# Performance work log

Hardware: AMD Instinct MI355X
Metric: run time of the kernel (lower is better)

## Reference

```python
import jax, jax.numpy as jnp
import numpy as np

NVAR, B, C, H, W = 3, 4, 256, 64, 64
C1 = C // 2          # dat channels (nc)
C2 = C - C1
HEADS = 4
HC = C1 // HEADS     # head channels
STRIDE = 4
KS = 4
HK, WK = H // STRIDE, W // STRIDE
NS = HK * WK         # n_sample
RPE_H, RPE_W = 2 * H - 1, 2 * W - 1
NPAIR = 3


def _grid_sample(img, grid):
    # img [B,C,Hi,Wi]; grid [B,Hg,Wg,2] = (x,y) in [-1,1]; bilinear, align_corners=True, zero-pad
    Bn, Cn, Hi, Wi = img.shape
    x = (grid[..., 0] + 1.0) * 0.5 * (Wi - 1)
    y = (grid[..., 1] + 1.0) * 0.5 * (Hi - 1)
    x0 = jnp.floor(x)
    y0 = jnp.floor(y)
    wx = x - x0
    wy = y - y0
    x0i = x0.astype(jnp.int32)
    y0i = y0.astype(jnp.int32)
    imt = img.transpose(0, 2, 3, 1)  # [B,Hi,Wi,C]
    bidx = jnp.arange(Bn)[:, None, None]

    def corner(yi, xi, wgt):
        ok = ((xi >= 0) & (xi < Wi) & (yi >= 0) & (yi < Hi)).astype(img.dtype)
        val = imt[bidx, jnp.clip(yi, 0, Hi - 1), jnp.clip(xi, 0, Wi - 1)]  # [B,Hg,Wg,C]
        return val * (wgt * ok)[..., None]

    out = (corner(y0i, x0i, (1 - wx) * (1 - wy))
           + corner(y0i, x0i + 1, wx * (1 - wy))
           + corner(y0i + 1, x0i, (1 - wx) * wy)
           + corner(y0i + 1, x0i + 1, wx * wy))
    return out.transpose(0, 3, 1, 2)  # [B,C,Hg,Wg]


def _ref_points(hk, wk):
    # normalized sampling-grid reference points, (y,x) order
    ry = (jnp.linspace(0.5, hk - 0.5, hk) / (hk - 1.0)) * 2.0 - 1.0
    rx = (jnp.linspace(0.5, wk - 0.5, wk) / (wk - 1.0)) * 2.0 - 1.0
    return jnp.stack(jnp.meshgrid(ry, rx, indexing='ij'), axis=-1)  # [hk,wk,2]


def _q_grid(h, w):
    gy = (jnp.arange(h, dtype=jnp.float32) / (h - 1.0)) * 2.0 - 1.0
    gx = (jnp.arange(w, dtype=jnp.float32) / (w - 1.0)) * 2.0 - 1.0
    return jnp.stack(jnp.meshgrid(gy, gx, indexing='ij'), axis=-1).reshape(h * w, 2)


def _conv1x1(x, w, b=None):
    y = jnp.einsum('oc,bchw->bohw', w, x)
    return y if b is None else y + b[None, :, None, None]


def _dat_block(q_in, kv_in, pWq, pbq, pWk, pbk, pWv, pbv, pWo, pbo,
               pdw_w, pdw_b, pln_g, pln_b, ppw_w, prpe):
    Bn = q_in.shape[0]
    q = _conv1x1(q_in, pWq, pbq)  # [B,C1,H,W]
    # offset net: depthwise 4x4 stride-4 conv -> channel LN -> GELU -> 1x1 conv to 2
    off = jax.lax.conv_general_dilated(
        q, pdw_w, (STRIDE, STRIDE), 'VALID',
        dimension_numbers=('NCHW', 'OIHW', 'NCHW'),
        feature_group_count=C1) + pdw_b[None, :, None, None]  # [B,C1,HK,WK]
    mu = off.mean(axis=1, keepdims=True)
    var = ((off - mu) ** 2).mean(axis=1, keepdims=True)
    off = (off - mu) * jax.lax.rsqrt(var + 1e-5) * pln_g[None, :, None, None] + pln_b[None, :, None, None]
    off = jax.nn.gelu(off, approximate=False)
    offset = _conv1x1(off, ppw_w).transpose(0, 2, 3, 1)  # [B,HK,WK,2] (dy,dx)
    # offset_range_factor = -1 -> no tanh scaling, clamp pos into [-1,1]
    pos = jnp.clip(offset + _ref_points(HK, WK)[None], -1.0, 1.0)  # [B,HK,WK,2]
    xs = _grid_sample(kv_in, pos[..., ::-1])  # sample kv at deformed points -> [B,C1,HK,WK]
    k = _conv1x1(xs, pWk, pbk).reshape(Bn, HEADS, HC, NS)
    v = _conv1x1(xs, pWv, pbv).reshape(Bn, HEADS, HC, NS)
    qh = q.reshape(Bn, HEADS, HC, H * W)
    attn = jnp.einsum('bhcm,bhcn->bhmn', qh, k) * (HC ** -0.5)  # [B,h,HW,NS]
    # relative position bias sampled from rpe table
    disp = (_q_grid(H, W)[None, :, None, :] - pos.reshape(Bn, 1, NS, 2)) * 0.5  # [B,HW,NS,2]
    rpe_b = jnp.broadcast_to(prpe[None], (Bn, HEADS, RPE_H, RPE_W))
    bias = _grid_sample(rpe_b, disp[..., ::-1])  # [B,h,HW,NS]
    attn = jax.nn.softmax(attn + bias, axis=-1)
    out = jnp.einsum('bhmn,bhcn->bhcm', attn, v).reshape(Bn, C1, H, W)
    return _conv1x1(out, pWo, pbo)


def _forward(xs, params):
    results = []
    num = 0
    for i in range(NVAR):
        res = xs[i]
        for j in range(i):
            attn_out = _dat_block(xs[i][:, :C1], xs[j][:, :C1],
                                  *(p[num] for p in params))
            # torch: res -= -cat(zeros[:,:C2], attn)  => add attn on channels C2:
            res = res.at[:, C2:].add(attn_out)
            num += 1
        results.append(res)
    return jnp.stack(results)  # [NVAR,B,C,H,W]


def setup_inputs() -> dict:
    key = jax.random.key(0)
    ks = jax.random.split(key, 4)
    d = {}
    for n, k in zip(['x0', 'x1', 'x2'], jax.random.split(ks[0], 3)):
        d[n] = jax.random.normal(k, (B, C, H, W), jnp.float32)

    def w(k, shape, s=0.02):
        return jax.random.normal(k, shape, jnp.float32) * s

    kk = jax.random.split(ks[1], 8)
    d['Wq'] = w(kk[0], (NPAIR, C1, C1))
    d['bq'] = jnp.zeros((NPAIR, C1), jnp.float32)
    d['Wk'] = w(kk[1], (NPAIR, C1, C1))
    d['bk'] = jnp.zeros((NPAIR, C1), jnp.float32)
    d['Wv'] = w(kk[2], (NPAIR, C1, C1))
    d['bv'] = jnp.zeros((NPAIR, C1), jnp.float32)
    d['Wo'] = w(kk[3], (NPAIR, C1, C1))
    d['bo'] = jnp.zeros((NPAIR, C1), jnp.float32)
    d['dw_w'] = w(kk[4], (NPAIR, C1, 1, KS, KS), 0.1)
    d['dw_b'] = jnp.zeros((NPAIR, C1), jnp.float32)
    d['ln_g'] = jnp.ones((NPAIR, C1), jnp.float32)
    d['ln_b'] = jnp.zeros((NPAIR, C1), jnp.float32)
    d['pw_w'] = w(kk[5], (NPAIR, 2, C1), 0.1)
    d['rpe'] = w(kk[6], (NPAIR, HEADS, RPE_H, RPE_W), 0.01)
    return d


def reference(x0, x1, x2, Wq, bq, Wk, bk, Wv, bv, Wo, bo,
              dw_w, dw_b, ln_g, ln_b, pw_w, rpe):
    params = (Wq, bq, Wk, bk, Wv, bv, Wo, bo, dw_w, dw_b, ln_g, ln_b, pw_w, rpe)
    out = _forward([x0, x1, x2], params)
    flow = jnp.zeros((NVAR, x0.shape[0]), out.dtype)
    return out, flow
```

## Files before the change

### kernel.cpp

```cpp
#include <hip/hip_runtime.h>
#include <math.h>

#define NVAR 3
#define BB 4
#define CC 256
#define C1 128
#define HEADS 4
#define HH 64
#define WW 64
#define HW 4096
#define RPE_W 127
#define NP 3
#define SCALE 0.17677669529663687f

typedef short bf16x8 __attribute__((ext_vector_type(8)));
typedef float f32x4 __attribute__((ext_vector_type(4)));
typedef __bf16 bf16x2 __attribute__((ext_vector_type(2)));

__device__ __forceinline__ unsigned short f2bf(float f) {
    unsigned int u = __float_as_uint(f);
    u += 0x7fffu + ((u >> 16) & 1u);
    return (unsigned short)(u >> 16);
}
__device__ __forceinline__ float bflo(unsigned u) { return __uint_as_float(u << 16); }
__device__ __forceinline__ float bfhi(unsigned u) { return __uint_as_float(u & 0xffff0000u); }

__device__ __forceinline__ float dot2bf(unsigned a, unsigned b, float c) {
#if __has_builtin(__builtin_amdgcn_fdot2_f32_bf16)
    return __builtin_amdgcn_fdot2_f32_bf16(__builtin_bit_cast(bf16x2, a),
                                           __builtin_bit_cast(bf16x2, b), c, false);
#else
    return c + bflo(a) * bflo(b) + bfhi(a) * bfhi(b);
#endif
}

__global__ __launch_bounds__(256) void prep_copy(const float* __restrict__ rpe,
                                                 const float* __restrict__ Wq,
                                                 const float* __restrict__ Wo,
                                                 const float* __restrict__ Wk,
                                                 const float* __restrict__ Wv,
                                                 const float* __restrict__ x0,
                                                 unsigned short* __restrict__ tabbf,
                                                 unsigned short* __restrict__ wqh,
                                                 unsigned short* __restrict__ woh,
                                                 unsigned short* __restrict__ wkh,
                                                 unsigned short* __restrict__ wvh,
                                                 float* __restrict__ out) {
    int blk = blockIdx.x;
    if (blk >= 24) {
        const long long n4 = (long long)BB * CC * HW / 4;
        long long i = (long long)(blk - 24) * 256 + threadIdx.x;
        const long long stride = 1024LL * 256;
        for (; i < n4 + 12; i += stride) {
            if (i < n4) ((float4*)out)[i] = ((const float4*)x0)[i];
            else out[3LL * BB * CC * HW + (i - n4)] = 0.f;
        }
        return;
    }
    if (blk < 12) {
        const float* src = rpe + (long long)blk * RPE_W * RPE_W;
        unsigned short* dst = tabbf + (long long)blk * 16384;
        for (int idx = threadIdx.x; idx < 16384; idx += 256) {
            int y = idx >> 7, x = idx & 127;
            float v = (y < RPE_W && x < RPE_W) ? src[y * RPE_W + x] : 0.f;
            dst[idx] = f2bf(v);
        }
    } else if (blk < 15) {
        int p = blk - 12;
        for (int i = threadIdx.x; i < 16384; i += 256)
            wqh[p * 16384 + i] = f2bf(Wq[p * 16384 + i]);
    } else if (blk < 18) {
        int p = blk - 15;
        for (int i = threadIdx.x; i < 16384; i += 256)
            woh[p * 16384 + i] = f2bf(Wo[p * 16384 + i]);
    } else if (blk < 21) {
        int p = blk - 18;
        for (int i = threadIdx.x; i < 16384; i += 256)
            wkh[p * 16384 + i] = f2bf(Wk[p * 16384 + i]);
    } else {
        int p = blk - 21;
        for (int i = threadIdx.x; i < 16384; i += 256)
            wvh[p * 16384 + i] = f2bf(Wv[p * 16384 + i]);
    }
}

__global__ __launch_bounds__(256) void conv_q(const float* __restrict__ x1,
                                              const float* __restrict__ x2,
                                              const unsigned short* __restrict__ wqh,
                                              const float* __restrict__ bq,
                                              unsigned short* __restrict__ qbf,
                                              float* __restrict__ out) {
    __shared__ unsigned short qlds[4][16][136];
    int wid = threadIdx.x >> 6, lane = threadIdx.x & 63;
    int g = lane >> 4, lm = lane & 15;
    int gw = blockIdx.x * 4 + wid;
    int mt = gw & 255;
    int pbi = gw >> 8;
    int merged = pbi >> 2;
    int b = pbi & 3;
    const float* X = (merged ? x2 : x1) + (long long)b * CC * HW;
    int m = mt * 16 + lm;
    int qi = merged + 1;
    float* outc = out + (((long long)(qi * 4 + b)) * CC) * HW + m;

    bf16x8 bh[4];
#pragma unroll
    for (int ksl = 0; ksl < 4; ksl++) {
        float v[8];
#pragma unroll
        for (int j = 0; j < 8; j++) {
            int k = ksl * 32 + 8 * g + j;
            v[j] = X[(long long)k * HW + m];
            outc[(long long)k * HW] = v[j];
        }
        union { unsigned u[4]; bf16x8 v; } H;
#pragma unroll
        for (int t = 0; t < 4; t++)
            H.u[t] = (unsigned)f2bf(v[2 * t]) | ((unsigned)f2bf(v[2 * t + 1]) << 16);
        bh[ksl] = H.v;
    }

    f32x4 zero = {0.f, 0.f, 0.f, 0.f};
    unsigned short* ql = &qlds[wid][lm][0];
    int qq = lane >> 4, cg = lane & 15;

    for (int rep = 0; rep <= merged; rep++) {
        int p = merged ? (1 + rep) : 0;
        int pb = p * 4 + b;
        const unsigned short* WH = wqh + p * 16384;
#pragma unroll
        for (int ct2 = 0; ct2 < 4; ct2++) {
            int ct0 = 2 * ct2, ct1 = ct0 + 1;
            f32x4 a0 = zero, a1 = zero;
#pragma unroll
            for (int ksl = 0; ksl < 4; ksl++) {
                bf16x8 Ah0 = *(const bf16x8*)(WH + (ct0 * 16 + lm) * 128 + ksl * 32 + 8 * g);
                bf16x8 Ah1 = *(const bf16x8*)(WH + (ct1 * 16 + lm) * 128 + ksl * 32 + 8 * g);
                a0 = __builtin_amdgcn_mfma_f32_16x16x32_bf16(Ah0, bh[ksl], a0, 0, 0, 0);
                a1 = __builtin_amdgcn_mfma_f32_16x16x32_bf16(Ah1, bh[ksl], a1, 0, 0, 0);
            }
            float q0[4], q1[4];
#pragma unroll
            for (int r = 0; r < 4; r++) {
                q0[r] = a0[r] + bq[p * 128 + ct0 * 16 + 4 * g + r];
                q1[r] = a1[r] + bq[p * 128 + ct1 * 16 + 4 * g + r];
            }
            *(unsigned*)(ql + ct0 * 16 + 4 * g) =
                (unsigned)f2bf(q0[0] * SCALE) | ((unsigned)f2bf(q0[1] * SCALE) << 16);
            *(unsigned*)(ql + ct0 * 16 + 4 * g + 2) =
                (unsigned)f2bf(q0[2] * SCALE) | ((unsigned)f2bf(q0[3] * SCALE) << 16);
            *(unsigned*)(ql + ct1 * 16 + 4 * g) =
                (unsigned)f2bf(q1[0] * SCALE) | ((unsigned)f2bf(q1[1] * SCALE) << 16);
            *(unsigned*)(ql + ct1 * 16 + 4 * g + 2) =
                (unsigned)f2bf(q1[2] * SCALE) | ((unsigned)f2bf(q1[3] * SCALE) << 16);
        }
        unsigned short* Yb = qbf + ((long long)pb * HW + mt * 16) * 128;
#pragma unroll
        for (int i = 0; i < 4; i++) {
            int row = i * 4 + qq;
            uint4 vv = *(const uint4*)&qlds[wid][row][cg * 8];
            *(uint4*)(Yb + row * 128 + cg * 8) = vv;
        }
    }
}

__global__ __launch_bounds__(256) void mid_kernel(const unsigned short* __restrict__ qbf,
                                                  const float* __restrict__ dw_w,
                                                  const float* __restrict__ dw_b,
                                                  const float* __restrict__ ln_g,
                                                  const float* __restrict__ ln_b,
                                                  const float* __restrict__ pw_w,
                                                  const float* __restrict__ x0,
                                                  const float* __restrict__ x1,
                                                  float* __restrict__ posb,
                                                  uint4* __restrict__ prmb,
                                                  unsigned short* __restrict__ xT) {
    __shared__ char sm[40960];
    int blk = blockIdx.x;
    int tid = threadIdx.x;
    if (blk < 192) {
        unsigned short* qs = (unsigned short*)sm;
        float (*dwout)[128] = (float(*)[128])(sm + 32768);
        int pb = blk >> 4, hk = blk & 15;
        int p = pb >> 2;
        int c = tid & 127;
        int wk0 = tid >> 7;
        const float* dwp_g = dw_w + (p * 128 + c) * 16;
        float dwp[16];
#pragma unroll
        for (int j = 0; j < 16; j++) dwp[j] = dwp_g[j] * (1.f / SCALE);
        float acc[8];
#pragma unroll
        for (int o = 0; o < 8; o++) acc[o] = dw_b[p * 128 + c];
        const unsigned short* Q = qbf + ((long long)pb * HW + hk * 256) * 128;
        for (int pass = 0; pass < 2; pass++) {
            __syncthreads();
#pragma unroll
            for (int it = 0; it < 8; it++) {
                int idx = tid + it * 256;
                int mloc = idx >> 4, cg = idx & 15;
                *(uint4*)(qs + mloc * 128 + cg * 8) =
                    *(const uint4*)(Q + (long long)(pass * 128 + mloc) * 128 + cg * 8);
            }
            __syncthreads();
#pragma unroll
            for (int o = 0; o < 8; o++) {
                int wk = wk0 + o * 2;
                float a = acc[o];
#pragma unroll
                for (int kyl = 0; kyl < 2; kyl++)
#pragma unroll
                    for (int kx = 0; kx < 4; kx++)
                        a += bflo((unsigned)qs[(kyl * 64 + wk * 4 + kx) * 128 + c])
                             * dwp[(pass * 2 + kyl) * 4 + kx];
                acc[o] = a;
            }
        }
        __syncthreads();
#pragma unroll
        for (int o = 0; o < 8; o++) dwout[wk0 + o * 2][c] = acc[o];
        __syncthreads();
        int wid = tid >> 6, lane = tid & 63;
        for (int i = 0; i < 4; i++) {
            int wk = wid * 4 + i;
            int s = hk * 16 + wk;
            float a0 = dwout[wk][lane], a1 = dwout[wk][lane + 64];
            float s1 = a0 + a1;
#pragma unroll
            for (int o = 1; o < 64; o <<= 1) s1 += __shfl_xor(s1, o);
            float mu = s1 * (1.f / 128.f);
            float d0 = a0 - mu, d1 = a1 - mu;
            float v2 = d0 * d0 + d1 * d1;
#pragma unroll
            for (int o = 1; o < 64; o <<= 1) v2 += __shfl_xor(v2, o);
            float rs = rsqrtf(v2 * (1.f / 128.f) + 1e-5f);
            int c0 = lane, c1 = lane + 64;
            float y0 = d0 * rs * ln_g[p * 128 + c0] + ln_b[p * 128 + c0];
            float y1 = d1 * rs * ln_g[p * 128 + c1] + ln_b[p * 128 + c1];
            float g0 = 0.5f * y0 * (1.f + erff(y0 * 0.70710678118654752f));
            float g1 = 0.5f * y1 * (1.f + erff(y1 * 0.70710678118654752f));
            float o0 = pw_w[(p * 2 + 0) * 128 + c0] * g0
                     + pw_w[(p * 2 + 0) * 128 + c1] * g1;
            float o1 = pw_w[(p * 2 + 1) * 128 + c0] * g0
                     + pw_w[(p * 2 + 1) * 128 + c1] * g1;
#pragma unroll
            for (int o = 1; o < 64; o <<= 1) o0 += __shfl_xor(o0, o);
#pragma unroll
            for (int o = 1; o < 64; o <<= 1) o1 += __shfl_xor(o1, o);
            if (lane == 0) {
                int wk2 = s & 15;
                float refy = (hk + 0.5f) * (2.f / 15.f) - 1.f;
                float refx = (wk2 + 0.5f) * (2.f / 15.f) - 1.f;
                float py = fminf(fmaxf(o0 + refy, -1.f), 1.f);
                float px = fminf(fmaxf(o1 + refx, -1.f), 1.f);
                int pbn = pb * 256 + s;
                posb[pbn * 2 + 0] = py;
                posb[pbn * 2 + 1] = px;
                float cy = 31.5f * (1.f - py), cx = 31.5f * (1.f - px);
                float yf = floorf(cy), xf = floorf(cx);
                float wy = cy - yf, wx = cx - xf;
                int Y0 = (int)yf, X0 = (int)xf;
                uint4 v;
                v.x = (unsigned)f2bf((1.f - wy) * (1.f - wx))
                    | ((unsigned)f2bf((1.f - wy) * wx) << 16);
                v.y = (unsigned)f2bf(wy * (1.f - wx))
                    | ((unsigned)f2bf(wy * wx) << 16);
                v.z = (unsigned)((Y0 * 128 + X0) * 2);
                v.w = 0;
                prmb[pbn] = v;
            }
        }
    } else {
        float (*ld2)[65] = (float(*)[65])sm;
        int rem = blk - 192;
        int v = rem >> 10;
        int rem1 = rem & 1023;
        int b = rem1 >> 8;
        int rem2 = rem1 & 255;
        int ct = rem2 >> 6;
        int mt = rem2 & 63;
        const float* src = ((v == 0) ? x0 : x1) + (long long)b * CC * HW
                           + (long long)(ct * 32) * HW + mt * 64;
#pragma unroll
        for (int it = 0; it < 2; it++) {
            int c = tid >> 3, x4 = (tid & 7) + it * 8;
            float4 w = *(const float4*)(src + (long long)c * HW + x4 * 4);
            ld2[c][x4 * 4 + 0] = w.x;
            ld2[c][x4 * 4 + 1] = w.y;
            ld2[c][x4 * 4 + 2] = w.z;
            ld2[c][x4 * 4 + 3] = w.w;
        }
        __syncthreads();
        int m = tid >> 2, cg = tid & 3;
        union { unsigned u[4]; } pk;
#pragma unroll
        for (int t = 0; t < 4; t++) {
            unsigned short h0 = f2bf(ld2[cg * 8 + 2 * t][m]);
            unsigned short h1 = f2bf(ld2[cg * 8 + 2 * t + 1][m]);
            pk.u[t] = (unsigned)h0 | ((unsigned)h1 << 16);
        }
        *(uint4*)(xT + (((long long)(v * 4 + b)) * HW + mt * 64 + m) * 128
                  + ct * 32 + cg * 8) = *(uint4*)pk.u;
    }
}

__global__ __launch_bounds__(256) void sample_kv(const unsigned short* __restrict__ xT,
                                                 const float* __restrict__ posb,
                                                 const unsigned short* __restrict__ wkh,
                                                 const unsigned short* __restrict__ wvh,
                                                 const float* __restrict__ bk,
                                                 const float* __restrict__ bv,
                                                 unsigned short* __restrict__ kbf,
                                                 unsigned short* __restrict__ vbf) {
    __shared__ unsigned short xls[32 * 128];
    int blk = blockIdx.x;
    int pb = blk >> 3;
    int nt = blk & 7;
    int p = pb >> 2, b = pb & 3;
    int n0 = nt * 32;
    int tid = threadIdx.x;

    {
        int nl = tid >> 3, co = tid & 7;
        int n = n0 + nl;
        float py = posb[(pb * 256 + n) * 2 + 0];
        float px = posb[(pb * 256 + n) * 2 + 1];
        float yi = (py + 1.f) * 31.5f, xi = (px + 1.f) * 31.5f;
        yi = fminf(fmaxf(yi, 0.f), 63.f);
        xi = fminf(fmaxf(xi, 0.f), 63.f);
        int y0 = min((int)yi, 62);
        int x0i = min((int)xi, 62);
        float wy = yi - (float)y0, wx = xi - (float)x0i;
        float w00 = (1.f - wy) * (1.f - wx), w01 = (1.f - wy) * wx;
        float w10 = wy * (1.f - wx), w11 = wy * wx;
        int vsel = (p == 2) ? 1 : 0;
        const unsigned short* base = xT + ((long long)(vsel * 4 + b)) * HW * 128;
        int m00 = y0 * 64 + x0i;
        char* dst = (char*)xls;
#pragma unroll
        for (int cb = 0; cb < 2; cb++) {
            int c0 = co * 16 + cb * 8;
            bf16x8 a = *(const bf16x8*)(base + (long long)m00 * 128 + c0);
            bf16x8 bb = *(const bf16x8*)(base + (long long)(m00 + 1) * 128 + c0);
            bf16x8 cc = *(const bf16x8*)(base + (long long)(m00 + 64) * 128 + c0);
            bf16x8 dd = *(const bf16x8*)(base + (long long)(m00 + 65) * 128 + c0);
            union { unsigned u[4]; bf16x8 v; } R;
#pragma unroll
            for (int t = 0; t < 4; t++) {
                float r0 = w00 * bflo((unsigned)(unsigned short)a[2 * t])
                         + w01 * bflo((unsigned)(unsigned short)bb[2 * t])
                         + w10 * bflo((unsigned)(unsigned short)cc[2 * t])
                         + w11 * bflo((unsigned)(unsigned short)dd[2 * t]);
                float r1 = w00 * bflo((unsigned)(unsigned short)a[2 * t + 1])
                         + w01 * bflo((unsigned)(unsigned short)bb[2 * t + 1])
                         + w10 * bflo((unsigned)(unsigned short)cc[2 * t + 1])
                         + w11 * bflo((unsigned)(unsigned short)dd[2 * t + 1]);
                R.u[t] = (unsigned)f2bf(r0) | ((unsigned)f2bf(r1) << 16);
            }
            *(bf16x8*)(dst + ((nl * 256 + c0 * 2) ^ ((nl & 7) << 4))) = R.v;
        }
    }
    __syncthreads();

    int wid = tid >> 6, lane = tid & 63;
    int g = lane >> 4, lm = lane & 15;
    int ntile = wid & 1, isv = wid >> 1;
    int nl = ntile * 16 + lm;
    const char* srcl = (const char*)xls;
    bf16x8 xf[4];
#pragma unroll
    for (int ks = 0; ks < 4; ks++)
        xf[ks] = *(const bf16x8*)(srcl + ((nl * 256 + (ks * 32 + 8 * g) * 2)
                                          ^ ((nl & 7) << 4)));
    f32x4 zero = {0.f, 0.f, 0.f, 0.f};
    if (!isv) {
        const unsigned short* WK = wkh + p * 16384;
#pragma unroll
        for (int ct = 0; ct < 8; ct++) {
            f32x4 acc = zero;
#pragma unroll
            for (int ks = 0; ks < 4; ks++) {
                bf16x8 wf = *(const bf16x8*)(WK + (ct * 16 + lm) * 128 + ks * 32 + 8 * g);
                acc = __builtin_amdgcn_mfma_f32_16x16x32_bf16(xf[ks], wf, acc, 0, 0, 0);
            }
            float bias = bk[p * 128 + ct * 16 + lm];
#pragma unroll
            for (int r = 0; r < 4; r++) {
                int n = n0 + ntile * 16 + 4 * g + r;
                kbf[((long long)pb * 256 + n) * 128 + ct * 16 + lm] = f2bf(acc[r] + bias);
            }
        }
    } else {
        const unsigned short* WV = wvh + p * 16384;
#pragma unroll
        for (int ct = 0; ct < 8; ct++) {
            f32x4 acc = zero;
#pragma unroll
            for (int ks = 0; ks < 4; ks++) {
                bf16x8 wf = *(const bf16x8*)(WV + (ct * 16 + lm) * 128 + ks * 32 + 8 * g);
                acc = __builtin_amdgcn_mfma_f32_16x16x32_bf16(wf, xf[ks], acc, 0, 0, 0);
            }
#pragma unroll
            for (int r = 0; r < 4; r++) {
                int c = ct * 16 + 4 * g + r;
                vbf[((long long)pb * 128 + c) * 256 + n0 + ntile * 16 + lm]
                    = f2bf(acc[r] + bv[p * 128 + c]);
            }
        }
    }
}

__global__ __launch_bounds__(512, 4) void attn_mfma(
        const unsigned short* __restrict__ qbf,
        const unsigned short* __restrict__ kbf,
        const unsigned short* __restrict__ vbf,
        const unsigned short* __restrict__ tabbf,
        const uint4* __restrict__ prmb,
        unsigned short* __restrict__ obf) {
    __shared__ unsigned short tab[16384 + 8];
    __shared__ uint4 prm[256];
    int tid = threadIdx.x;
    int wid = tid >> 6, lane = tid & 63;
    int g = lane >> 4, lm = lane & 15;
    int nh = wid >> 2;
    int mq = wid & 3;
    int bid = blockIdx.x;
    int my = bid & 63;
    int h = (bid >> 6) & 3;
    int b = (bid >> 8) & 3;
    int p = bid >> 10;
    int pb = p * 4 + b;

    {
        const uint4* ts = (const uint4*)(tabbf + (long long)(p * 4 + h) * 16384);
        uint4* td = (uint4*)tab;
#pragma unroll
        for (int i = 0; i < 4; i++) td[tid + i * 512] = ts[tid + i * 512];
        if (tid < 256) prm[tid] = prmb[pb * 256 + tid];
    }
    __syncthreads();

    int mx = (mq << 4) + lm;
    int nb = nh * 128;

    bf16x8 qf = *(const bf16x8*)(qbf + ((long long)pb * HW + my * 64 + mx) * 128
                                 + h * 32 + 8 * g);
    const unsigned short* kbase = kbf + ((long long)pb * 256 + lm) * 128
                                  + h * 32 + 8 * g;
    f32x4 zero = {0.f, 0.f, 0.f, 0.f};
    f32x4 acc[8];
    __builtin_amdgcn_s_setprio(1);
#pragma unroll
    for (int ni = 0; ni < 8; ni++) {
        bf16x8 kf = *(const bf16x8*)(kbase + (nb + ni * 16) * 128);
        acc[ni] = __builtin_amdgcn_mfma_f32_16x16x32_bf16(kf, qf, zero, 0, 0, 0);
    }
    __builtin_amdgcn_s_setprio(0);

    int laneoff = (my * 128 + mx) * 2;
    const char* tb = (const char*)tab;
#pragma unroll
    for (int ni = 0; ni < 8; ni++) {
#pragma unroll
        for (int r = 0; r < 4; r++) {
            int n = nb + ni * 16 + 4 * g + r;
            uint4 pw = prm[n];
            int va = (int)pw.z + laneoff;
            int va4 = va & ~3;
            int sh = va & 3;
            unsigned r0 = *(const unsigned*)(tb + va4);
            unsigned r1 = *(const unsigned*)(tb + va4 + 4);
            unsigned r2 = *(const unsigned*)(tb + va4 + 256);
            unsigned r3 = *(const unsigned*)(tb + va4 + 260);
            unsigned p0 = __builtin_amdgcn_alignbyte(r1, r0, sh);
            unsigned p1 = __builtin_amdgcn_alignbyte(r3, r2, sh);
            float t = acc[ni][r];
            t = dot2bf(p0, pw.x, t);
            t = dot2bf(p1, pw.y, t);
            acc[ni][r] = t;
        }
    }

    float mloc = -1e30f;
#pragma unroll
    for (int ni = 0; ni < 8; ni++)
        mloc = fmaxf(mloc, fmaxf(fmaxf(acc[ni][0], acc[ni][1]),
                                 fmaxf(acc[ni][2], acc[ni][3])));
    mloc = fmaxf(mloc, __shfl_xor(mloc, 16));
    mloc = fmaxf(mloc, __shfl_xor(mloc, 32));

    float* mex = (float*)tab;
    float* sex = (float*)tab + 128;
    float* oex = (float*)tab + 256;
    __syncthreads();
    if (g == 0) mex[nh * 64 + mx] = mloc;
    __syncthreads();
    float mglob = fmaxf(mex[mx], mex[64 + mx]);

    float lsum = 0.f;
    unsigned dwA[8], dwB[8];
#pragma unroll
    for (int ni = 0; ni < 8; ni++) {
        float e0 = __expf(acc[ni][0] - mglob);
        float e1 = __expf(acc[ni][1] - mglob);
        float e2 = __expf(acc[ni][2] - mglob);
        float e3 = __expf(acc[ni][3] - mglob);
        lsum += (e0 + e1) + (e2 + e3);
        asm("v_cvt_pk_bf16_f32 %0, %1, %2" : "=v"(dwA[ni]) : "v"(e0), "v"(e1));
        asm("v_cvt_pk_bf16_f32 %0, %1, %2" : "=v"(dwB[ni]) : "v"(e2), "v"(e3));
    }
    lsum += __shfl_xor(lsum, 16);
    lsum += __shfl_xor(lsum, 32);
    if (g == 0) sex[nh * 64 + mx] = lsum;

    int src0 = ((g & 1) << 5) + lm;
    int src1 = src0 + 16;
    bool sel = (g >> 1) != 0;
    const unsigned short* vb0 = vbf + ((long long)pb * 128 + h * 32 + lm) * 256
                                + 8 * g + nb;
    f32x4 o0 = zero, o1 = zero;
#pragma unroll
    for (int st = 0; st < 4; st++) {
        unsigned d0a = __shfl(dwA[2 * st], src0), d0b = __shfl(dwA[2 * st + 1], src0);
        unsigned d1a = __shfl(dwB[2 * st], src0), d1b = __shfl(dwB[2 * st + 1], src0);
        unsigned d2a = __shfl(dwA[2 * st], src1), d2b = __shfl(dwA[2 * st + 1], src1);
        unsigned d3a = __shfl(dwB[2 * st], src1), d3b = __shfl(dwB[2 * st + 1], src1);
        union { unsigned u[4]; bf16x8 v; } pf;
        pf.u[0] = sel ? d0b : d0a;
        pf.u[1] = sel ? d1b : d1a;
        pf.u[2] = sel ? d2b : d2a;
        pf.u[3] = sel ? d3b : d3a;
        bf16x8 v0 = *(const bf16x8*)(vb0 + st * 32);
        bf16x8 v1 = *(const bf16x8*)(vb0 + 4096 + st * 32);
        __builtin_amdgcn_s_setprio(1);
        o0 = __builtin_amdgcn_mfma_f32_16x16x32_bf16(v0, pf.v, o0, 0, 0, 0);
        o1 = __builtin_amdgcn_mfma_f32_16x16x32_bf16(v1, pf.v, o1, 0, 0, 0);
        __builtin_amdgcn_s_setprio(0);
    }

    if (nh == 1) {
        float* od = oex + (mq * 64 + lane) * 8;
#pragma unroll
        for (int r = 0; r < 4; r++) { od[r] = o0[r]; od[4 + r] = o1[r]; }
    }
    __syncthreads();
    if (nh == 1) return;

    const float* os = oex + (mq * 64 + lane) * 8;
#pragma unroll
    for (int r = 0; r < 4; r++) { o0[r] += os[r]; o1[r] += os[4 + r]; }
    float inv = 1.f / (sex[mx] + sex[64 + mx]);

    unsigned short* bounce = tab + 6144;
    {
        unsigned short* rw = bounce + mq * 640 + lm * 40;
        *(unsigned*)(rw + g * 4) =
            (unsigned)f2bf(o0[0] * inv) | ((unsigned)f2bf(o0[1] * inv) << 16);
        *(unsigned*)(rw + g * 4 + 2) =
            (unsigned)f2bf(o0[2] * inv) | ((unsigned)f2bf(o0[3] * inv) << 16);
        *(unsigned*)(rw + 16 + g * 4) =
            (unsigned)f2bf(o1[0] * inv) | ((unsigned)f2bf(o1[1] * inv) << 16);
        *(unsigned*)(rw + 16 + g * 4 + 2) =
            (unsigned)f2bf(o1[2] * inv) | ((unsigned)f2bf(o1[3] * inv) << 16);
    }
    int row = lane >> 2, cb = lane & 3;
    uint4 vv = *(const uint4*)(bounce + mq * 640 + row * 40 + cb * 8);
    *(uint4*)(obf + ((long long)pb * HW + my * 64 + mq * 16 + row) * 128
              + h * 32 + cb * 8) = vv;
}

__global__ __launch_bounds__(256) void conv_wo(const float* __restrict__ x1,
                                               const float* __restrict__ x2,
                                               const unsigned short* __restrict__ obf,
                                               const unsigned short* __restrict__ woh,
                                               const float* __restrict__ bo,
                                               float* __restrict__ out) {
    int wid = threadIdx.x >> 6, lane = threadIdx.x & 63;
    int g = lane >> 4, lm = lane & 15;
    int gw = blockIdx.x * 4 + wid;
    int mt = gw & 255;
    int b = (gw >> 8) & 3;
    int vs = gw >> 10;
    int m = mt * 16 + lm;
    int np = vs + 1;

    f32x4 acc[8];
#pragma unroll
    for (int ct = 0; ct < 8; ct++) acc[ct] = (f32x4){0.f, 0.f, 0.f, 0.f};

    for (int pi = 0; pi < np; pi++) {
        int p = vs ? (1 + pi) : 0;
        const unsigned short* Om = obf + ((long long)(p * 4 + b) * HW + m) * 128;
        const unsigned short* WH = woh + p * 16384;
#pragma unroll
        for (int ksl = 0; ksl < 4; ksl++) {
            bf16x8 bh = *(const bf16x8*)(Om + ksl * 32 + 8 * g);
#pragma unroll
            for (int ct = 0; ct < 8; ct++) {
                bf16x8 A = *(const bf16x8*)(WH + (ct * 16 + lm) * 128 + ksl * 32 + 8 * g);
                acc[ct] = __builtin_amdgcn_mfma_f32_16x16x32_bf16(A, bh, acc[ct], 0, 0, 0);
            }
        }
    }

    int qi = vs + 1;
    const float* xq = (vs ? x2 : x1) + (long long)b * CC * HW;
#pragma unroll
    for (int ct = 0; ct < 8; ct++)
#pragma unroll
        for (int r = 0; r < 4; r++) {
            int c = ct * 16 + 4 * g + r;
            float bias = vs ? (bo[128 + c] + bo[256 + c]) : bo[c];
            float base = xq[(long long)(128 + c) * HW + m];
            out[(((long long)(qi * 4 + b)) * CC + 128 + c) * HW + m]
                = base + acc[ct][r] + bias;
        }
}

extern "C" void kernel_launch(void* const* d_in, const int* in_sizes, int n_in,
                              void* d_out, int out_size, void* d_ws, size_t ws_size,
                              hipStream_t stream) {
    const float* x0 = (const float*)d_in[0];
    const float* x1 = (const float*)d_in[1];
    const float* x2 = (const float*)d_in[2];
    const float* Wq = (const float*)d_in[3];
    const float* bq = (const float*)d_in[4];
    const float* Wk = (const float*)d_in[5];
    const float* bk = (const float*)d_in[6];
    const float* Wv = (const float*)d_in[7];
    const float* bv = (const float*)d_in[8];
    const float* Wo = (const float*)d_in[9];
    const float* bo = (const float*)d_in[10];
    const float* dw_w = (const float*)d_in[11];
    const float* dw_b = (const float*)d_in[12];
    const float* ln_g = (const float*)d_in[13];
    const float* ln_b = (const float*)d_in[14];
    const float* pw_w = (const float*)d_in[15];
    const float* rpe = (const float*)d_in[16];
    float* out = (float*)d_out;

    float* ws = (float*)d_ws;
    unsigned short* obf = (unsigned short*)ws;
    float* posb = ws + 6291456;
    unsigned short* xT = (unsigned short*)(posb + 6144);
    unsigned short* qbf = xT + 4194304;
    unsigned short* kbf = qbf + 12582912;
    unsigned short* vbf = kbf + 393216;
    unsigned short* tabbf = vbf + 393216;
    uint4* prmb = (uint4*)(tabbf + 196608);
    unsigned short* wqh = (unsigned short*)(prmb + 3072);
    unsigned short* woh = wqh + 49152;
    unsigned short* wkh = woh + 49152;
    unsigned short* wvh = wkh + 49152;

    prep_copy<<<1048, 256, 0, stream>>>(rpe, Wq, Wo, Wk, Wv, x0, tabbf,
                                        wqh, woh, wkh, wvh, out);
    conv_q<<<512, 256, 0, stream>>>(x1, x2, wqh, bq, qbf, out);
    mid_kernel<<<2240, 256, 0, stream>>>(qbf, dw_w, dw_b, ln_g, ln_b, pw_w,
                                         x0, x1, posb, prmb, xT);
    sample_kv<<<96, 256, 0, stream>>>(xT, posb, wkh, wvh, bk, bv, kbf, vbf);
    attn_mfma<<<3072, 512, 0, stream>>>(qbf, kbf, vbf, tabbf, prmb, obf);
    conv_wo<<<512, 256, 0, stream>>>(x1, x2, obf, woh, bo, out);
}
```

Baseline: 161.5 us.

## Pack vertically adjacent RPE rows into 32-bit table entries for bilinear gather

The relative position bias table is re-laid out so each 32-bit entry holds the bf16 values at row y and row y+1. The attention kernel now loads only the 64-row slice it needs into shared memory. Each bilinear lookup becomes two aligned 32-bit LDS reads instead of four reads plus two alignbyte shuffles, and the bilinear weight packing is reordered to match. This cuts LDS traffic and ALU work in the score loop, at the cost of a table twice as large in global memory and an extra read per element in prep.

```diff
diff --git a/kernel.cpp b/kernel.cpp
--- a/kernel.cpp
+++ b/kernel.cpp
@@ -40,7 +40,7 @@
                                                  const float* __restrict__ Wk,
                                                  const float* __restrict__ Wv,
                                                  const float* __restrict__ x0,
-                                                 unsigned short* __restrict__ tabbf,
+                                                 unsigned* __restrict__ dtabbf,
                                                  unsigned short* __restrict__ wqh,
                                                  unsigned short* __restrict__ woh,
                                                  unsigned short* __restrict__ wkh,
@@ -59,11 +59,12 @@
     }
     if (blk < 12) {
         const float* src = rpe + (long long)blk * RPE_W * RPE_W;
-        unsigned short* dst = tabbf + (long long)blk * 16384;
+        unsigned* dst = dtabbf + (long long)blk * 16384;
         for (int idx = threadIdx.x; idx < 16384; idx += 256) {
             int y = idx >> 7, x = idx & 127;
-            float v = (y < RPE_W && x < RPE_W) ? src[y * RPE_W + x] : 0.f;
-            dst[idx] = f2bf(v);
+            float v0 = (y < RPE_W && x < RPE_W) ? src[y * RPE_W + x] : 0.f;
+            float v1 = (y + 1 < RPE_W && x < RPE_W) ? src[(y + 1) * RPE_W + x] : 0.f;
+            dst[idx] = (unsigned)f2bf(v0) | ((unsigned)f2bf(v1) << 16);
         }
     } else if (blk < 15) {
         int p = blk - 12;
@@ -262,10 +263,10 @@
                 int Y0 = (int)yf, X0 = (int)xf;
                 uint4 v;
                 v.x = (unsigned)f2bf((1.f - wy) * (1.f - wx))
-                    | ((unsigned)f2bf((1.f - wy) * wx) << 16);
-                v.y = (unsigned)f2bf(wy * (1.f - wx))
+                    | ((unsigned)f2bf(wy * (1.f - wx)) << 16);
+                v.y = (unsigned)f2bf((1.f - wy) * wx)
                     | ((unsigned)f2bf(wy * wx) << 16);
-                v.z = (unsigned)((Y0 * 128 + X0) * 2);
+                v.z = (unsigned)((Y0 * 128 + X0) * 4);
                 v.w = 0;
                 prmb[pbn] = v;
             }
@@ -414,10 +415,10 @@
         const unsigned short* __restrict__ qbf,
         const unsigned short* __restrict__ kbf,
         const unsigned short* __restrict__ vbf,
-        const unsigned short* __restrict__ tabbf,
+        const unsigned* __restrict__ dtabbf,
         const uint4* __restrict__ prmb,
         unsigned short* __restrict__ obf) {
-    __shared__ unsigned short tab[16384 + 8];
+    __shared__ unsigned tab[64 * 128 + 4];
     __shared__ uint4 prm[256];
     int tid = threadIdx.x;
     int wid = tid >> 6, lane = tid & 63;
@@ -432,7 +433,8 @@
     int pb = p * 4 + b;
 
     {
-        const uint4* ts = (const uint4*)(tabbf + (long long)(p * 4 + h) * 16384);
+        const uint4* ts = (const uint4*)(dtabbf + (long long)(p * 4 + h) * 16384
+                                         + my * 128);
         uint4* td = (uint4*)tab;
 #pragma unroll
         for (int i = 0; i < 4; i++) td[tid + i * 512] = ts[tid + i * 512];
@@ -457,7 +459,7 @@
     }
     __builtin_amdgcn_s_setprio(0);
 
-    int laneoff = (my * 128 + mx) * 2;
+    int laneoff = mx * 4;
     const char* tb = (const char*)tab;
 #pragma unroll
     for (int ni = 0; ni < 8; ni++) {
@@ -466,17 +468,11 @@
             int n = nb + ni * 16 + 4 * g + r;
             uint4 pw = prm[n];
             int va = (int)pw.z + laneoff;
-            int va4 = va & ~3;
-            int sh = va & 3;
-            unsigned r0 = *(const unsigned*)(tb + va4);
-            unsigned r1 = *(const unsigned*)(tb + va4 + 4);
-            unsigned r2 = *(const unsigned*)(tb + va4 + 256);
-            unsigned r3 = *(const unsigned*)(tb + va4 + 260);
-            unsigned p0 = __builtin_amdgcn_alignbyte(r1, r0, sh);
-            unsigned p1 = __builtin_amdgcn_alignbyte(r3, r2, sh);
+            unsigned d0 = *(const unsigned*)(tb + va);
+            unsigned d1 = *(const unsigned*)(tb + va + 4);
             float t = acc[ni][r];
-            t = dot2bf(p0, pw.x, t);
-            t = dot2bf(p1, pw.y, t);
+            t = dot2bf(d0, pw.x, t);
+            t = dot2bf(d1, pw.y, t);
             acc[ni][r] = t;
         }
     }
@@ -551,7 +547,7 @@
     for (int r = 0; r < 4; r++) { o0[r] += os[r]; o1[r] += os[4 + r]; }
     float inv = 1.f / (sex[mx] + sex[64 + mx]);
 
-    unsigned short* bounce = tab + 6144;
+    unsigned short* bounce = (unsigned short*)tab + 4608;
     {
         unsigned short* rw = bounce + mq * 640 + lm * 40;
         *(unsigned*)(rw + g * 4) =
@@ -646,19 +642,19 @@
     unsigned short* qbf = xT + 4194304;
     unsigned short* kbf = qbf + 12582912;
     unsigned short* vbf = kbf + 393216;
-    unsigned short* tabbf = vbf + 393216;
-    uint4* prmb = (uint4*)(tabbf + 196608);
+    unsigned* dtabbf = (unsigned*)(vbf + 393216);
+    uint4* prmb = (uint4*)(dtabbf + 196608);
     unsigned short* wqh = (unsigned short*)(prmb + 3072);
     unsigned short* woh = wqh + 49152;
     unsigned short* wkh = woh + 49152;
     unsigned short* wvh = wkh + 49152;
 
-    prep_copy<<<1048, 256, 0, stream>>>(rpe, Wq, Wo, Wk, Wv, x0, tabbf,
+    prep_copy<<<1048, 256, 0, stream>>>(rpe, Wq, Wo, Wk, Wv, x0, dtabbf,
                                         wqh, woh, wkh, wvh, out);
     conv_q<<<512, 256, 0, stream>>>(x1, x2, wqh, bq, qbf, out);
     mid_kernel<<<2240, 256, 0, stream>>>(qbf, dw_w, dw_b, ln_g, ln_b, pw_w,
                                          x0, x1, posb, prmb, xT);
     sample_kv<<<96, 256, 0, stream>>>(xT, posb, wkh, wvh, bk, bv, kbf, vbf);
-    attn_mfma<<<3072, 512, 0, stream>>>(qbf, kbf, vbf, tabbf, prmb, obf);
+    attn_mfma<<<3072, 512, 0, stream>>>(qbf, kbf, vbf, dtabbf, prmb, obf);
     conv_wo<<<512, 256, 0, stream>>>(x1, x2, obf, woh, bo, out);
 }
```

After: 160.3 us. Within noise of the previous version (-0.8%).
